# Performance work log

Hardware: AMD Instinct MI355X
Metric: run time of the kernel (lower is better)

Reference implementation:

```python
import jax, jax.numpy as jnp
import numpy as np

N_AGENTS = 10000
N_TARGETS = 10000
N_EDGES = 320000
IN_CH = 8
DS = 32          # n_channels // 2 per GAT preprocessor
NCH = 64         # n_channels
C = 128          # 2 * n_channels hidden width
OUT = 2
N_TAPS = 3
N_LAYERS = 2
RADIUS = 2.0
K_NBR = 10       # max_num_neighbors in radius_graph
BIG = 1e9


def radius_nbrs(qpos, kpos, radius, k, exclude_self):
    """For each query point, indices of <=k nearest key points within radius."""
    d2 = jnp.sum((qpos[:, None, :] - kpos[None, :, :]) ** 2, axis=-1)  # [Nq, Nk]
    if exclude_self:
        n = qpos.shape[0]
        d2 = d2.at[jnp.arange(n), jnp.arange(n)].set(BIG)
    d2 = jnp.where(d2 <= radius * radius, d2, BIG)
    negv, idx = jax.lax.top_k(-d2, k)   # nearest-k (deterministic stand-in for PyG's first-k)
    valid = negv > -BIG * 0.5           # [Nq, k] True where a real in-radius neighbor
    return idx, valid


def gatv2(src_feats, dst_feats, idx, valid, Wl, Wr, att, b):
    """Single-head GATv2Conv over a fixed-K neighbor list (idx indexes src_feats)."""
    xl = src_feats @ Wl                      # [Ns, H] messages
    xr = dst_feats @ Wr                      # [Nd, H]
    g = jax.nn.leaky_relu(xl[idx] + xr[:, None, :], 0.2)   # [Nd, K, H]
    s = jnp.einsum('nkh,h->nk', g, att)
    s = jnp.where(valid, s, -BIG)
    s = s - jnp.max(s, axis=1, keepdims=True)
    p = jnp.exp(s) * valid                   # masked exp; isolated nodes -> all-zero
    alpha = p / (jnp.sum(p, axis=1, keepdims=True) + 1e-16)
    return jnp.einsum('nk,nkh->nh', alpha, xl[idx]) + b


def graph_filter(x, src, dst, W, b, n):
    """Polynomial graph filter: y = sum_k S^k x W_k + b, S = unweighted adjacency."""
    y = x @ W[0]
    h = x
    for k in range(1, W.shape[0]):
        h = jax.ops.segment_sum(h[src], dst, num_segments=n)  # one shift tap
        y = y + h @ W[k]
    return y + b


def setup_inputs() -> dict:
    key = jax.random.key(0)
    ks = jax.random.split(key, 16)
    f32 = jnp.float32
    return {
        'own_obs': jax.random.normal(ks[0], (N_AGENTS, IN_CH), dtype=f32),
        'agent_positions': jax.random.uniform(ks[1], (N_AGENTS, 2), dtype=f32) * 100.0,
        'target_positions': jax.random.uniform(ks[2], (N_TARGETS, 2), dtype=f32) * 100.0,
        'W_self': jax.random.normal(ks[3], (IN_CH, NCH), dtype=f32) * 0.1,
        'b_self': jnp.zeros((NCH,), f32),
        'ag_Wl': jax.random.normal(ks[4], (2, DS), dtype=f32) * 0.1,
        'ag_Wr': jax.random.normal(ks[5], (2, DS), dtype=f32) * 0.1,
        'ag_att': jax.random.normal(ks[6], (DS,), dtype=f32) * 0.1,
        'ag_b': jnp.zeros((DS,), f32),
        'tg_Wl': jax.random.normal(ks[7], (2, DS), dtype=f32) * 0.1,
        'tg_Wr': jax.random.normal(ks[8], (2, DS), dtype=f32) * 0.1,
        'tg_att': jax.random.normal(ks[9], (DS,), dtype=f32) * 0.1,
        'tg_b': jnp.zeros((DS,), f32),
        'gf_W': jax.random.normal(ks[10], (N_LAYERS, N_TAPS + 1, C, C), dtype=f32) * (1.0 / np.sqrt(C)),
        'gf_b': jnp.zeros((N_LAYERS, C), f32),
        'bn_gamma': jnp.ones((N_LAYERS, C), f32),
        'bn_beta': jnp.zeros((N_LAYERS, C), f32),
        'W_read': jax.random.normal(ks[11], (C, OUT), dtype=f32) * 0.1,
        'b_read': jnp.zeros((OUT,), f32),
        'edge_index': jax.random.randint(ks[12], (2, N_EDGES), 0, N_AGENTS, dtype=jnp.int32),
    }


def reference(own_obs, agent_positions, target_positions, W_self, b_self,
              ag_Wl, ag_Wr, ag_att, ag_b, tg_Wl, tg_Wr, tg_att, tg_b,
              gf_W, gf_b, bn_gamma, bn_beta, W_read, b_read, edge_index):
    n = agent_positions.shape[0]
    # dynamic radius graphs (agent-agent; target->agent)
    a_idx, a_valid = radius_nbrs(agent_positions, agent_positions, RADIUS, K_NBR, True)
    t_idx, t_valid = radius_nbrs(agent_positions, target_positions, RADIUS, K_NBR, False)

    s = own_obs @ W_self + b_self                                            # self MLP (1 layer)
    a = gatv2(agent_positions, agent_positions, a_idx, a_valid, ag_Wl, ag_Wr, ag_att, ag_b)
    t = gatv2(target_positions, agent_positions, t_idx, t_valid, tg_Wl, tg_Wr, tg_att, tg_b)
    x = jnp.concatenate([s, a, t], axis=1)                                   # [N, 128]

    src, dst = edge_index[0], edge_index[1]
    for l in range(N_LAYERS):
        h = graph_filter(x, src, dst, gf_W[l], gf_b[l], n)
        mu = jnp.mean(h, axis=0)
        var = jnp.var(h, axis=0)
        h = (h - mu) / jnp.sqrt(var + 1e-5) * bn_gamma[l] + bn_beta[l]       # BatchNorm
        x = x + jax.nn.leaky_relu(h, 0.01)                                   # residual block
    return x @ W_read + b_read
```

## Files before the change

kernel.cpp:

```cpp
#include <hip/hip_runtime.h>

typedef unsigned long long u64;
typedef unsigned int u32;
typedef unsigned short ushort_t;

#define NA 10000
#define NE 320000
#define KN 10
#define GRID 50
#define NCELL (GRID * GRID)
#define GATB 157

typedef __attribute__((ext_vector_type(8))) short short8v;
typedef __attribute__((ext_vector_type(4))) float f32x4;

__device__ __forceinline__ u32 f2bf(float f) {
  union { float f; u32 u; } v; v.f = f;
  return (v.u + 0x7fffu + ((v.u >> 16) & 1u)) >> 16;
}
__device__ __forceinline__ float bf2f(u32 b) {
  union { u32 u; float f; } v; v.u = b << 16;
  return v.f;
}

__device__ __forceinline__ void insert10(u64* top, u64 key) {
#pragma unroll
  for (int t = 9; t > 0; --t) {
    u64 prev = top[t - 1];
    u64 cur = top[t];
    top[t] = (key < prev) ? prev : ((key < cur) ? key : cur);
  }
  top[0] = (key < top[0]) ? key : top[0];
}

__device__ __forceinline__ int cell_of(float2 p) {
  int cx = (int)(p.x * 0.5f);
  int cy = (int)(p.y * 0.5f);
  cx = min(max(cx, 0), GRID - 1);
  cy = min(max(cy, 0), GRID - 1);
  return cy * GRID + cx;
}

__global__ __launch_bounds__(256) void k_zero_packw(int* __restrict__ deg, int* __restrict__ cur,
                                                    int* __restrict__ chist, int* __restrict__ ccur,
                                                    const float* __restrict__ gfW,
                                                    ushort_t* __restrict__ Wh, ushort_t* __restrict__ Wlo) {
  int i = blockIdx.x * 256 + threadIdx.x;
  if (i < NA) deg[i] = 0;
  else if (i < 2 * NA) cur[i - NA] = 0;
  else if (i < 2 * NA + 2 * NCELL) chist[i - 2 * NA] = 0;
  else if (i < 2 * NA + 4 * NCELL) ccur[i - 2 * NA - 2 * NCELL] = 0;
  if (i < 131072) {
    int l = i >> 16;
    int rem = i & 65535;
    int t = rem >> 14;
    int k = (rem >> 7) & 127;
    int n = rem & 127;
    float v = gfW[(size_t)i];
    int kt = k >> 5;
    int hi = (k >> 3) & 3;
    int j = k & 7;
    int ct = n >> 4;
    int lane = hi * 16 + (n & 15);
    size_t dst = (((((size_t)(l * 4 + t) * 4 + kt) * 8 + ct) * 64 + lane) * 8 + j);
    u32 h = f2bf(v);
    float r = v - bf2f(h);
    Wh[dst] = (ushort_t)h;
    Wlo[dst] = (ushort_t)f2bf(r);
  }
}

__global__ __launch_bounds__(256) void k_hist_self(const int* __restrict__ edst,
                                                   const float2* __restrict__ apos,
                                                   const float2* __restrict__ tpos,
                                                   int* __restrict__ deg, int* __restrict__ chist,
                                                   const float* __restrict__ own_obs,
                                                   const float* __restrict__ W_self, const float* __restrict__ b_self,
                                                   float* __restrict__ x) {
  __shared__ float sW[512], sb[64];
  int t = threadIdx.x;
  for (int i = t; i < 512; i += 256) sW[i] = W_self[i];
  if (t < 64) sb[t] = b_self[t];
  __syncthreads();
  int i = blockIdx.x * 256 + t;
  if (i < NE) {
    atomicAdd(&deg[edst[i]], 1);
  } else if (i < NE + 2 * NA) {
    int ii = i - NE;
    int graph = (ii >= NA) ? 1 : 0;
    int idx = ii - graph * NA;
    float2 p = graph ? tpos[idx] : apos[idx];
    atomicAdd(&chist[graph * NCELL + cell_of(p)], 1);
  } else if (i < NE + 2 * NA + 8 * NA) {
    int gid = i - NE - 2 * NA;
    int q = gid >> 3;
    int c8 = (gid & 7) * 8;
    const float4* op = (const float4*)(own_obs + (size_t)q * 8);
    float4 o0 = op[0], o1 = op[1];
    float obs[8] = {o0.x, o0.y, o0.z, o0.w, o1.x, o1.y, o1.z, o1.w};
    float out[8];
#pragma unroll
    for (int jj = 0; jj < 8; ++jj) {
      int c = c8 + jj;
      float s = sb[c];
#pragma unroll
      for (int k = 0; k < 8; ++k) s += obs[k] * sW[k * 64 + c];
      out[jj] = s;
    }
    float* xrow = x + (size_t)q * 128 + c8;
    *(float4*)(xrow) = make_float4(out[0], out[1], out[2], out[3]);
    *(float4*)(xrow + 4) = make_float4(out[4], out[5], out[6], out[7]);
  }
}

__global__ __launch_bounds__(1024) void k_scan_all(const int* __restrict__ deg, int* __restrict__ rp,
                                                   const int* __restrict__ chist, int* __restrict__ crp) {
  __shared__ int part[1024];
  int t = threadIdx.x;
  const int* in;
  int* out;
  int per, tot;
  if (blockIdx.x == 0) { in = deg; out = rp; per = 10; tot = NA; }
  else { in = chist; out = crp; per = 5; tot = 2 * NCELL; }
  int beg = min(t * per, tot), end = min(beg + per, tot);
  int s = 0;
  for (int i = beg; i < end; ++i) s += in[i];
  part[t] = s;
  __syncthreads();
  for (int o = 1; o < 1024; o <<= 1) {
    int v = part[t];
    int u = (t >= o) ? part[t - o] : 0;
    __syncthreads();
    part[t] = v + u;
    __syncthreads();
  }
  int base = (t > 0) ? part[t - 1] : 0;
  for (int i = beg; i < end; ++i) { out[i] = base; base += in[i]; }
  if (t == 1023) out[tot] = part[1023];
}

__global__ __launch_bounds__(256) void k_scatter_all(const int* __restrict__ esrc, const int* __restrict__ edst,
                                                     const int* __restrict__ rp, int* __restrict__ cur,
                                                     int* __restrict__ col,
                                                     const float2* __restrict__ apos, const float2* __restrict__ tpos,
                                                     const int* __restrict__ crp, int* __restrict__ ccur,
                                                     float2* __restrict__ ps, int* __restrict__ pid) {
  int i = blockIdx.x * 256 + threadIdx.x;
  if (i < NE) {
    int d = edst[i];
    int p = atomicAdd(&cur[d], 1);
    col[rp[d] + p] = esrc[i];
  } else if (i < NE + 2 * NA) {
    int ii = i - NE;
    int graph = (ii >= NA) ? 1 : 0;
    int idx = ii - graph * NA;
    float2 p = graph ? tpos[idx] : apos[idx];
    int gc = graph * NCELL + cell_of(p);
    int o = crp[gc] + atomicAdd(&ccur[gc], 1);
    ps[o] = p;
    pid[o] = idx;
  }
}

__global__ __launch_bounds__(256) void k_nbr2(const float2* __restrict__ apos,
                                              const int* __restrict__ rp,
                                              const float2* __restrict__ ps, const int* __restrict__ pid,
                                              int* __restrict__ a_idx, int* __restrict__ a_cnt,
                                              int* __restrict__ t_idx, int* __restrict__ t_cnt) {
  int tid = blockIdx.x * 256 + threadIdx.x;
  if (tid >= 2 * NA) return;
  int graph = (tid >= NA) ? 1 : 0;
  int q = tid - graph * NA;
  float2 qp = apos[q];
  int cx = min(max((int)(qp.x * 0.5f), 0), GRID - 1);
  int cy = min(max((int)(qp.y * 0.5f), 0), GRID - 1);

  u64 top[10];
#pragma unroll
  for (int t = 0; t < 10; ++t) top[t] = ~0ull;

  int x0 = max(cx - 1, 0), x1 = min(cx + 1, GRID - 1);
  int y0 = max(cy - 1, 0), y1 = min(cy + 1, GRID - 1);
  for (int yy = y0; yy <= y1; ++yy) {
    int cb = graph * NCELL + yy * GRID + x0;
    int ce = graph * NCELL + yy * GRID + x1;
    int b = rp[cb], e = rp[ce + 1];
    for (int j = b; j < e; ++j) {
      float2 kp = ps[j];
      float dx = qp.x - kp.x;
      float dy = qp.y - kp.y;
      float d2 = __fadd_rn(__fmul_rn(dx, dx), __fmul_rn(dy, dy));
      int g = pid[j];
      if (d2 <= 4.0f && !(graph == 0 && g == q)) {
        u64 key = ((u64)__float_as_uint(d2) << 32) | (u32)g;
        if (key < top[9]) insert10(top, key);
      }
    }
  }
  int cnt = 0;
#pragma unroll
  for (int t = 0; t < 10; ++t) cnt += (top[t] != ~0ull) ? 1 : 0;
  int* oi = graph ? t_idx : a_idx;
#pragma unroll
  for (int t = 0; t < 10; ++t) oi[(size_t)q * 10 + t] = (int)(u32)(top[t] & 0xffffffffu);
  if (graph) t_cnt[q] = cnt; else a_cnt[q] = cnt;
}

__global__ __launch_bounds__(64) void k_gat2(const float2* __restrict__ apos, const float2* __restrict__ tpos,
                                             const int* __restrict__ a_idx, const int* __restrict__ a_cnt,
                                             const int* __restrict__ t_idx, const int* __restrict__ t_cnt,
                                             const float* __restrict__ agWl, const float* __restrict__ agWr,
                                             const float* __restrict__ agatt, const float* __restrict__ agb,
                                             const float* __restrict__ tgWl, const float* __restrict__ tgWr,
                                             const float* __restrict__ tgatt, const float* __restrict__ tgb,
                                             float* __restrict__ x) {
  int graph = (blockIdx.x >= GATB) ? 1 : 0;
  int b0 = blockIdx.x - graph * GATB;
  const float2* srcpos = graph ? tpos : apos;
  const int* idx_all = graph ? t_idx : a_idx;
  const int* cnt_all = graph ? t_cnt : a_cnt;
  const float* Wl = graph ? tgWl : agWl;
  const float* Wr = graph ? tgWr : agWr;
  const float* att = graph ? tgatt : agatt;
  const float* bbp = graph ? tgb : agb;
  int outoff = graph ? 96 : 64;

  __shared__ float sWl[64], sWr[64], satt[32], sbb[32];
  int t = threadIdx.x;
  sWl[t] = Wl[t];
  sWr[t] = Wr[t];
  if (t < 32) { satt[t] = att[t]; sbb[t] = bbp[t]; }
  __syncthreads();
  int q = b0 * 64 + t;
  if (q >= NA) return;
  float2 qp = apos[q];
  float xr[32];
#pragma unroll
  for (int c = 0; c < 32; ++c) xr[c] = qp.x * sWr[c] + qp.y * sWr[32 + c];
  const int* il = idx_all + (size_t)q * 10;
  int cnt = cnt_all[q];
  int idx[10];
#pragma unroll
  for (int k = 0; k < 10; ++k) idx[k] = (k < cnt) ? il[k] : 0;
  float pv[10];
  float m = -1e30f;
#pragma unroll
  for (int k = 0; k < 10; ++k) {
    float2 p = srcpos[idx[k]];
    float s = 0.f;
#pragma unroll
    for (int c = 0; c < 32; ++c) {
      float xl = p.x * sWl[c] + p.y * sWl[32 + c];
      float g = xl + xr[c];
      g = (g >= 0.f) ? g : 0.2f * g;
      s += satt[c] * g;
    }
    pv[k] = s;
    m = (k < cnt) ? fmaxf(m, s) : m;
  }
  float sum = 0.f;
#pragma unroll
  for (int k = 0; k < 10; ++k) {
    float e = (k < cnt) ? expf(pv[k] - m) : 0.f;
    pv[k] = e;
    sum += e;
  }
  float inv = 1.f / (sum + 1e-16f);
  float out[32];
#pragma unroll
  for (int c = 0; c < 32; ++c) out[c] = sbb[c];
#pragma unroll
  for (int k = 0; k < 10; ++k) {
    float a = pv[k] * inv;
    float2 p = srcpos[idx[k]];
#pragma unroll
    for (int c = 0; c < 32; ++c) {
      float xl = p.x * sWl[c] + p.y * sWl[32 + c];
      out[c] += a * xl;
    }
  }
  float* xrow = x + (size_t)q * 128 + outoff;
#pragma unroll
  for (int c4 = 0; c4 < 8; ++c4)
    *(float4*)(xrow + c4 * 4) = make_float4(out[c4 * 4], out[c4 * 4 + 1], out[c4 * 4 + 2], out[c4 * 4 + 3]);
}

__global__ __launch_bounds__(256) void k_shift3(const float* __restrict__ xin, float* __restrict__ xout,
                                                const int* __restrict__ rp, const int* __restrict__ col) {
  int bid = blockIdx.x;
  int half = (bid & 7) >> 2;
  int slot = (bid >> 3) * 4 + (bid & 3);
  if (slot >= 625) return;
  int wid = threadIdx.x >> 6;
  int lane = threadIdx.x & 63;
  int q = lane >> 4;
  int li = lane & 15;
  int row = slot * 16 + wid * 4 + q;
  int beg = rp[row], end = rp[row + 1];
  const f32x4* x4 = (const f32x4*)xin;
  int base = half * 16 + li;
  f32x4 acc = {0.f, 0.f, 0.f, 0.f};
  int j = beg;
  for (; j + 1 < end; j += 2) {
    int s0 = col[j], s1 = col[j + 1];
    f32x4 v0 = x4[(size_t)s0 * 32 + base];
    f32x4 v1 = x4[(size_t)s1 * 32 + base];
    acc += v0;
    acc += v1;
  }
  if (j < end) acc += x4[(size_t)col[j] * 32 + base];
  __builtin_nontemporal_store(acc, &((f32x4*)xout)[(size_t)row * 32 + base]);
}

__global__ __launch_bounds__(256) void k_gemm_mfma3(const float* __restrict__ a0, const float* __restrict__ a1,
                                                    const float* __restrict__ a2, const float* __restrict__ a3,
                                                    const ushort_t* __restrict__ Wh, const ushort_t* __restrict__ Wlo,
                                                    const float* __restrict__ b, float* __restrict__ y,
                                                    double* __restrict__ parts) {
  const int lane = threadIdx.x & 63;
  const int wave = threadIdx.x >> 6;
  const int ct0 = wave * 2;
  const int row = lane & 15;
  const int hi = lane >> 4;
  const int rb = blockIdx.x * 16;

  f32x4 acc[2];
#pragma unroll
  for (int c = 0; c < 2; ++c) {
    float bv = b[(ct0 + c) * 16 + row];
    acc[c][0] = bv; acc[c][1] = bv; acc[c][2] = bv; acc[c][3] = bv;
  }

  const float* aps[4] = {a0, a1, a2, a3};
#pragma unroll
  for (int t = 0; t < 4; ++t) {
    const float* at = aps[t];
#pragma unroll
    for (int kt = 0; kt < 4; ++kt) {
      const float* ap = at + (size_t)(rb + row) * 128 + kt * 32 + hi * 8;
      float4 fa = *(const float4*)(ap);
      float4 fb = *(const float4*)(ap + 4);
      float av[8] = {fa.x, fa.y, fa.z, fa.w, fb.x, fb.y, fb.z, fb.w};
      short8v ah, al;
#pragma unroll
      for (int j = 0; j < 8; ++j) {
        u32 h = f2bf(av[j]);
        float r = av[j] - bf2f(h);
        ah[j] = (short)h;
        al[j] = (short)f2bf(r);
      }
#pragma unroll
      for (int c = 0; c < 2; ++c) {
        size_t widx = ((((size_t)t * 4 + kt) * 8 + (ct0 + c)) * 64 + lane) * 8;
        short8v bh = *(const short8v*)(Wh + widx);
        short8v bl = *(const short8v*)(Wlo + widx);
        acc[c] = __builtin_amdgcn_mfma_f32_16x16x32_bf16(ah, bh, acc[c], 0, 0, 0);
        acc[c] = __builtin_amdgcn_mfma_f32_16x16x32_bf16(al, bh, acc[c], 0, 0, 0);
        acc[c] = __builtin_amdgcn_mfma_f32_16x16x32_bf16(ah, bl, acc[c], 0, 0, 0);
      }
    }
  }

#pragma unroll
  for (int c = 0; c < 2; ++c) {
#pragma unroll
    for (int r = 0; r < 4; ++r) {
      int grow = rb + hi * 4 + r;
      y[(size_t)grow * 128 + (ct0 + c) * 16 + row] = acc[c][r];
    }
  }

#pragma unroll
  for (int c = 0; c < 2; ++c) {
    double s = 0.0, ss = 0.0;
#pragma unroll
    for (int r = 0; r < 4; ++r) {
      double v = (double)acc[c][r];
      s += v;
      ss += v * v;
    }
    s += __shfl_xor(s, 16);
    ss += __shfl_xor(ss, 16);
    s += __shfl_xor(s, 32);
    ss += __shfl_xor(ss, 32);
    if (hi == 0) {
      int ch = (ct0 + c) * 16 + row;
      parts[(size_t)ch * 625 + blockIdx.x] = s;
      parts[(size_t)(128 + ch) * 625 + blockIdx.x] = ss;
    }
  }
}

__global__ __launch_bounds__(256) void k_bnfin(const double* __restrict__ parts,
                                               const float* __restrict__ gamma, const float* __restrict__ beta,
                                               float* __restrict__ AB) {
  __shared__ double s0[256], s1[256];
  int ch = blockIdx.x;
  int t = threadIdx.x;
  const double* ps = parts + (size_t)ch * 625;
  const double* pq = parts + (size_t)(128 + ch) * 625;
  double a = 0.0, b = 0.0;
  for (int i = t; i < 625; i += 256) { a += ps[i]; b += pq[i]; }
  s0[t] = a;
  s1[t] = b;
  __syncthreads();
  for (int o = 128; o > 0; o >>= 1) {
    if (t < o) { s0[t] += s0[t + o]; s1[t] += s1[t + o]; }
    __syncthreads();
  }
  if (t == 0) {
    double mu = s0[0] / (double)NA;
    double var = s1[0] / (double)NA - mu * mu;
    double rs = 1.0 / sqrt(var + 1e-5);
    AB[ch] = (float)rs * gamma[ch];
    AB[128 + ch] = beta[ch] - (float)(mu * rs) * gamma[ch];
  }
}

__global__ __launch_bounds__(256) void k_bnapply(const float* __restrict__ y, const float* __restrict__ AB,
                                                 const float* __restrict__ Wread, const float* __restrict__ bread,
                                                 float* __restrict__ x, float* __restrict__ out, int doread) {
  __shared__ float sAB[256], sWr[256];
  int t = threadIdx.x;
  sAB[t] = AB[t];
  sWr[t] = Wread[t];
  __syncthreads();
  const int n4 = NA * 32;
  for (int i = blockIdx.x * 256 + t; i < n4; i += gridDim.x * 256) {
    float4 yv = ((const float4*)y)[i];
    int c = (i & 31) * 4;
    float v0 = yv.x * sAB[c + 0] + sAB[128 + c + 0];
    float v1 = yv.y * sAB[c + 1] + sAB[128 + c + 1];
    float v2 = yv.z * sAB[c + 2] + sAB[128 + c + 2];
    float v3 = yv.w * sAB[c + 3] + sAB[128 + c + 3];
    v0 = (v0 >= 0.f) ? v0 : 0.01f * v0;
    v1 = (v1 >= 0.f) ? v1 : 0.01f * v1;
    v2 = (v2 >= 0.f) ? v2 : 0.01f * v2;
    v3 = (v3 >= 0.f) ? v3 : 0.01f * v3;
    float4 xv = ((float4*)x)[i];
    xv.x += v0; xv.y += v1; xv.z += v2; xv.w += v3;
    ((float4*)x)[i] = xv;
    if (doread) {
      float a0 = xv.x * sWr[(c + 0) * 2] + xv.y * sWr[(c + 1) * 2] + xv.z * sWr[(c + 2) * 2] + xv.w * sWr[(c + 3) * 2];
      float a1 = xv.x * sWr[(c + 0) * 2 + 1] + xv.y * sWr[(c + 1) * 2 + 1] + xv.z * sWr[(c + 2) * 2 + 1] + xv.w * sWr[(c + 3) * 2 + 1];
#pragma unroll
      for (int o = 1; o < 32; o <<= 1) {
        a0 += __shfl_xor(a0, o);
        a1 += __shfl_xor(a1, o);
      }
      if ((i & 31) == 0) {
        int row = i >> 5;
        out[row * 2 + 0] = a0 + bread[0];
        out[row * 2 + 1] = a1 + bread[1];
      }
    }
  }
}

extern "C" void kernel_launch(void* const* d_in, const int* in_sizes, int n_in,
                              void* d_out, int out_size, void* d_ws, size_t ws_size,
                              hipStream_t stream) {
  (void)in_sizes; (void)n_in; (void)out_size; (void)ws_size;
  const float* own_obs = (const float*)d_in[0];
  const float2* apos = (const float2*)d_in[1];
  const float2* tpos = (const float2*)d_in[2];
  const float* W_self = (const float*)d_in[3];
  const float* b_self = (const float*)d_in[4];
  const float* agWl = (const float*)d_in[5];
  const float* agWr = (const float*)d_in[6];
  const float* agatt = (const float*)d_in[7];
  const float* agb = (const float*)d_in[8];
  const float* tgWl = (const float*)d_in[9];
  const float* tgWr = (const float*)d_in[10];
  const float* tgatt = (const float*)d_in[11];
  const float* tgb = (const float*)d_in[12];
  const float* gfW = (const float*)d_in[13];
  const float* gfb = (const float*)d_in[14];
  const float* bng = (const float*)d_in[15];
  const float* bnb = (const float*)d_in[16];
  const float* Wread = (const float*)d_in[17];
  const float* bread = (const float*)d_in[18];
  const int* ei = (const int*)d_in[19];
  const int* esrc = ei;
  const int* edst = ei + NE;

  char* w = (char*)d_ws;
  size_t off = 0;
  auto take = [&](size_t bytes) -> void* {
    void* p = w + off;
    off += (bytes + 255) & ~(size_t)255;
    return p;
  };
  int* a_idx = (int*)take((size_t)NA * KN * 4);
  int* t_idx = (int*)take((size_t)NA * KN * 4);
  int* a_cnt = (int*)take((size_t)NA * 4);
  int* t_cnt = (int*)take((size_t)NA * 4);
  float* x = (float*)take((size_t)NA * 128 * 4);
  float* y = (float*)take((size_t)NA * 128 * 4);
  float* sh1 = (float*)take((size_t)NA * 128 * 4);
  float* sh2 = (float*)take((size_t)NA * 128 * 4);
  float* sh3 = (float*)take((size_t)NA * 128 * 4);
  ushort_t* Wh = (ushort_t*)take((size_t)131072 * 2);
  ushort_t* Wlo = (ushort_t*)take((size_t)131072 * 2);
  double* parts = (double*)take((size_t)256 * 625 * 8);
  float* AB = (float*)take(256 * 4);
  int* deg = (int*)take((size_t)NA * 4);
  int* cur = (int*)take((size_t)NA * 4);
  int* rp = (int*)take((size_t)(NA + 1) * 4);
  int* col = (int*)take((size_t)NE * 4);
  int* chist = (int*)take((size_t)2 * NCELL * 4);
  int* crp = (int*)take((size_t)(2 * NCELL + 1) * 4);
  int* ccur = (int*)take((size_t)2 * NCELL * 4);
  float2* ps = (float2*)take((size_t)2 * NA * 8);
  int* pid = (int*)take((size_t)2 * NA * 4);

  k_zero_packw<<<131072 / 256, 256, 0, stream>>>(deg, cur, chist, ccur, gfW, Wh, Wlo);
  k_hist_self<<<(NE + 2 * NA + 8 * NA + 255) / 256, 256, 0, stream>>>(edst, apos, tpos, deg, chist,
                                                                      own_obs, W_self, b_self, x);
  k_scan_all<<<2, 1024, 0, stream>>>(deg, rp, chist, crp);
  k_scatter_all<<<(NE + 2 * NA + 255) / 256, 256, 0, stream>>>(esrc, edst, rp, cur, col,
                                                               apos, tpos, crp, ccur, ps, pid);
  k_nbr2<<<(2 * NA + 255) / 256, 256, 0, stream>>>(apos, crp, ps, pid, a_idx, a_cnt, t_idx, t_cnt);
  k_gat2<<<2 * GATB, 64, 0, stream>>>(apos, tpos, a_idx, a_cnt, t_idx, t_cnt,
                                      agWl, agWr, agatt, agb, tgWl, tgWr, tgatt, tgb, x);

  for (int l = 0; l < 2; ++l) {
    const ushort_t* Whl = Wh + (size_t)l * 65536;
    const ushort_t* Wll = Wlo + (size_t)l * 65536;
    const float* bl = gfb + (size_t)l * 128;
    const float* gl = bng + (size_t)l * 128;
    const float* bb = bnb + (size_t)l * 128;
    k_shift3<<<1256, 256, 0, stream>>>(x, sh1, rp, col);
    k_shift3<<<1256, 256, 0, stream>>>(sh1, sh2, rp, col);
    k_shift3<<<1256, 256, 0, stream>>>(sh2, sh3, rp, col);
    k_gemm_mfma3<<<NA / 16, 256, 0, stream>>>(x, sh1, sh2, sh3, Whl, Wll, bl, y, parts);
    k_bnfin<<<128, 256, 0, stream>>>(parts, gl, bb, AB);
    k_bnapply<<<256, 256, 0, stream>>>(y, AB, Wread, bread, x, (float*)d_out, l == 1 ? 1 : 0);
  }
}
```

Before: 251.2 us.

## Fuse neighbor search with GATv2 and degree-sort rows for SpMM shifts

Merges the radius-neighbor search kernel and the GATv2 attention kernel into one, keeping the top-10 neighbor indices in registers so the a_idx/t_idx/cnt buffers are never written or read back. It also builds a degree-bucketed row permutation (histogram in a third scan block, scatter in the scatter kernel) so the sparse shift kernels process rows of similar degree together and reduce wave divergence. The shift inner loop is unrolled to four gathers per iteration. The permutation costs extra atomics and an indirect row lookup, and the fused kernel uses more registers, which may lower occupancy.

```diff
diff --git a/kernel.cpp b/kernel.cpp
--- a/kernel.cpp
+++ b/kernel.cpp
@@ -9,7 +9,6 @@
 #define KN 10
 #define GRID 50
 #define NCELL (GRID * GRID)
-#define GATB 157
 
 typedef __attribute__((ext_vector_type(8))) short short8v;
 typedef __attribute__((ext_vector_type(4))) float f32x4;
@@ -43,6 +42,7 @@
 
 __global__ __launch_bounds__(256) void k_zero_packw(int* __restrict__ deg, int* __restrict__ cur,
                                                     int* __restrict__ chist, int* __restrict__ ccur,
+                                                    int* __restrict__ dcur,
                                                     const float* __restrict__ gfW,
                                                     ushort_t* __restrict__ Wh, ushort_t* __restrict__ Wlo) {
   int i = blockIdx.x * 256 + threadIdx.x;
@@ -50,6 +50,7 @@
   else if (i < 2 * NA) cur[i - NA] = 0;
   else if (i < 2 * NA + 2 * NCELL) chist[i - 2 * NA] = 0;
   else if (i < 2 * NA + 4 * NCELL) ccur[i - 2 * NA - 2 * NCELL] = 0;
+  else if (i < 2 * NA + 4 * NCELL + 128) dcur[i - 2 * NA - 4 * NCELL] = 0;
   if (i < 131072) {
     int l = i >> 16;
     int rem = i & 65535;
@@ -114,9 +115,22 @@
 }
 
 __global__ __launch_bounds__(1024) void k_scan_all(const int* __restrict__ deg, int* __restrict__ rp,
-                                                   const int* __restrict__ chist, int* __restrict__ crp) {
+                                                   const int* __restrict__ chist, int* __restrict__ crp,
+                                                   int* __restrict__ dbase) {
+  int t = threadIdx.x;
+  if (blockIdx.x == 2) {
+    __shared__ int dh[128];
+    if (t < 128) dh[t] = 0;
+    __syncthreads();
+    for (int i = t; i < NA; i += 1024) atomicAdd(&dh[min(deg[i], 127)], 1);
+    __syncthreads();
+    if (t == 0) {
+      int run = 0;
+      for (int b = 0; b < 128; ++b) { int c = dh[b]; dbase[b] = run; run += c; }
+    }
+    return;
+  }
   __shared__ int part[1024];
-  int t = threadIdx.x;
   const int* in;
   int* out;
   int per, tot;
@@ -144,7 +158,9 @@
                                                      int* __restrict__ col,
                                                      const float2* __restrict__ apos, const float2* __restrict__ tpos,
                                                      const int* __restrict__ crp, int* __restrict__ ccur,
-                                                     float2* __restrict__ ps, int* __restrict__ pid) {
+                                                     float2* __restrict__ ps, int* __restrict__ pid,
+                                                     const int* __restrict__ deg, const int* __restrict__ dbase,
+                                                     int* __restrict__ dcur, int* __restrict__ perm) {
   int i = blockIdx.x * 256 + threadIdx.x;
   if (i < NE) {
     int d = edst[i];
@@ -159,15 +175,31 @@
     int o = crp[gc] + atomicAdd(&ccur[gc], 1);
     ps[o] = p;
     pid[o] = idx;
-  }
-}
-
-__global__ __launch_bounds__(256) void k_nbr2(const float2* __restrict__ apos,
-                                              const int* __restrict__ rp,
-                                              const float2* __restrict__ ps, const int* __restrict__ pid,
-                                              int* __restrict__ a_idx, int* __restrict__ a_cnt,
-                                              int* __restrict__ t_idx, int* __restrict__ t_cnt) {
-  int tid = blockIdx.x * 256 + threadIdx.x;
+  } else if (i < NE + 2 * NA + NA) {
+    int r = i - NE - 2 * NA;
+    int b = min(deg[r], 127);
+    int pos = atomicAdd(&dcur[b], 1);
+    perm[dbase[b] + pos] = r;
+  }
+}
+
+__global__ __launch_bounds__(256) void k_nbr_gat(const float2* __restrict__ apos, const float2* __restrict__ tpos,
+                                                 const int* __restrict__ crp,
+                                                 const float2* __restrict__ ps, const int* __restrict__ pid,
+                                                 const float* __restrict__ agWl, const float* __restrict__ agWr,
+                                                 const float* __restrict__ agatt, const float* __restrict__ agb,
+                                                 const float* __restrict__ tgWl, const float* __restrict__ tgWr,
+                                                 const float* __restrict__ tgatt, const float* __restrict__ tgb,
+                                                 float* __restrict__ x) {
+  __shared__ float sWl[2][64], sWr[2][64], satt[2][32], sbb[2][32];
+  int t = threadIdx.x;
+  if (t < 64) { sWl[0][t] = agWl[t]; sWr[0][t] = agWr[t]; sWl[1][t] = tgWl[t]; sWr[1][t] = tgWr[t]; }
+  else if (t < 96) {
+    int u = t - 64;
+    satt[0][u] = agatt[u]; sbb[0][u] = agb[u]; satt[1][u] = tgatt[u]; sbb[1][u] = tgb[u];
+  }
+  __syncthreads();
+  int tid = blockIdx.x * 256 + t;
   if (tid >= 2 * NA) return;
   int graph = (tid >= NA) ? 1 : 0;
   int q = tid - graph * NA;
@@ -177,14 +209,14 @@
 
   u64 top[10];
 #pragma unroll
-  for (int t = 0; t < 10; ++t) top[t] = ~0ull;
+  for (int k = 0; k < 10; ++k) top[k] = ~0ull;
 
   int x0 = max(cx - 1, 0), x1 = min(cx + 1, GRID - 1);
   int y0 = max(cy - 1, 0), y1 = min(cy + 1, GRID - 1);
   for (int yy = y0; yy <= y1; ++yy) {
     int cb = graph * NCELL + yy * GRID + x0;
     int ce = graph * NCELL + yy * GRID + x1;
-    int b = rp[cb], e = rp[ce + 1];
+    int b = crp[cb], e = crp[ce + 1];
     for (int j = b; j < e; ++j) {
       float2 kp = ps[j];
       float dx = qp.x - kp.x;
@@ -199,49 +231,19 @@
   }
   int cnt = 0;
 #pragma unroll
-  for (int t = 0; t < 10; ++t) cnt += (top[t] != ~0ull) ? 1 : 0;
-  int* oi = graph ? t_idx : a_idx;
-#pragma unroll
-  for (int t = 0; t < 10; ++t) oi[(size_t)q * 10 + t] = (int)(u32)(top[t] & 0xffffffffu);
-  if (graph) t_cnt[q] = cnt; else a_cnt[q] = cnt;
-}
-
-__global__ __launch_bounds__(64) void k_gat2(const float2* __restrict__ apos, const float2* __restrict__ tpos,
-                                             const int* __restrict__ a_idx, const int* __restrict__ a_cnt,
-                                             const int* __restrict__ t_idx, const int* __restrict__ t_cnt,
-                                             const float* __restrict__ agWl, const float* __restrict__ agWr,
-                                             const float* __restrict__ agatt, const float* __restrict__ agb,
-                                             const float* __restrict__ tgWl, const float* __restrict__ tgWr,
-                                             const float* __restrict__ tgatt, const float* __restrict__ tgb,
-                                             float* __restrict__ x) {
-  int graph = (blockIdx.x >= GATB) ? 1 : 0;
-  int b0 = blockIdx.x - graph * GATB;
+  for (int k = 0; k < 10; ++k) cnt += (top[k] != ~0ull) ? 1 : 0;
+  int idx[10];
+#pragma unroll
+  for (int k = 0; k < 10; ++k) idx[k] = (k < cnt) ? (int)(u32)(top[k] & 0xffffffffu) : 0;
+
   const float2* srcpos = graph ? tpos : apos;
-  const int* idx_all = graph ? t_idx : a_idx;
-  const int* cnt_all = graph ? t_cnt : a_cnt;
-  const float* Wl = graph ? tgWl : agWl;
-  const float* Wr = graph ? tgWr : agWr;
-  const float* att = graph ? tgatt : agatt;
-  const float* bbp = graph ? tgb : agb;
-  int outoff = graph ? 96 : 64;
-
-  __shared__ float sWl[64], sWr[64], satt[32], sbb[32];
-  int t = threadIdx.x;
-  sWl[t] = Wl[t];
-  sWr[t] = Wr[t];
-  if (t < 32) { satt[t] = att[t]; sbb[t] = bbp[t]; }
-  __syncthreads();
-  int q = b0 * 64 + t;
-  if (q >= NA) return;
-  float2 qp = apos[q];
+  const float* wl = sWl[graph];
+  const float* wr = sWr[graph];
+  const float* at = satt[graph];
+  const float* bb = sbb[graph];
   float xr[32];
 #pragma unroll
-  for (int c = 0; c < 32; ++c) xr[c] = qp.x * sWr[c] + qp.y * sWr[32 + c];
-  const int* il = idx_all + (size_t)q * 10;
-  int cnt = cnt_all[q];
-  int idx[10];
-#pragma unroll
-  for (int k = 0; k < 10; ++k) idx[k] = (k < cnt) ? il[k] : 0;
+  for (int c = 0; c < 32; ++c) xr[c] = qp.x * wr[c] + qp.y * wr[32 + c];
   float pv[10];
   float m = -1e30f;
 #pragma unroll
@@ -250,10 +252,10 @@
     float s = 0.f;
 #pragma unroll
     for (int c = 0; c < 32; ++c) {
-      float xl = p.x * sWl[c] + p.y * sWl[32 + c];
+      float xl = p.x * wl[c] + p.y * wl[32 + c];
       float g = xl + xr[c];
       g = (g >= 0.f) ? g : 0.2f * g;
-      s += satt[c] * g;
+      s += at[c] * g;
     }
     pv[k] = s;
     m = (k < cnt) ? fmaxf(m, s) : m;
@@ -268,25 +270,26 @@
   float inv = 1.f / (sum + 1e-16f);
   float out[32];
 #pragma unroll
-  for (int c = 0; c < 32; ++c) out[c] = sbb[c];
+  for (int c = 0; c < 32; ++c) out[c] = bb[c];
 #pragma unroll
   for (int k = 0; k < 10; ++k) {
     float a = pv[k] * inv;
     float2 p = srcpos[idx[k]];
 #pragma unroll
     for (int c = 0; c < 32; ++c) {
-      float xl = p.x * sWl[c] + p.y * sWl[32 + c];
+      float xl = p.x * wl[c] + p.y * wl[32 + c];
       out[c] += a * xl;
     }
   }
-  float* xrow = x + (size_t)q * 128 + outoff;
+  float* xrow = x + (size_t)q * 128 + (graph ? 96 : 64);
 #pragma unroll
   for (int c4 = 0; c4 < 8; ++c4)
     *(float4*)(xrow + c4 * 4) = make_float4(out[c4 * 4], out[c4 * 4 + 1], out[c4 * 4 + 2], out[c4 * 4 + 3]);
 }
 
 __global__ __launch_bounds__(256) void k_shift3(const float* __restrict__ xin, float* __restrict__ xout,
-                                                const int* __restrict__ rp, const int* __restrict__ col) {
+                                                const int* __restrict__ rp, const int* __restrict__ col,
+                                                const int* __restrict__ perm) {
   int bid = blockIdx.x;
   int half = (bid & 7) >> 2;
   int slot = (bid >> 3) * 4 + (bid & 3);
@@ -295,20 +298,24 @@
   int lane = threadIdx.x & 63;
   int q = lane >> 4;
   int li = lane & 15;
-  int row = slot * 16 + wid * 4 + q;
+  int row = perm[slot * 16 + wid * 4 + q];
   int beg = rp[row], end = rp[row + 1];
   const f32x4* x4 = (const f32x4*)xin;
   int base = half * 16 + li;
   f32x4 acc = {0.f, 0.f, 0.f, 0.f};
   int j = beg;
-  for (; j + 1 < end; j += 2) {
-    int s0 = col[j], s1 = col[j + 1];
+  for (; j + 3 < end; j += 4) {
+    int s0 = col[j], s1 = col[j + 1], s2 = col[j + 2], s3 = col[j + 3];
     f32x4 v0 = x4[(size_t)s0 * 32 + base];
     f32x4 v1 = x4[(size_t)s1 * 32 + base];
+    f32x4 v2 = x4[(size_t)s2 * 32 + base];
+    f32x4 v3 = x4[(size_t)s3 * 32 + base];
     acc += v0;
     acc += v1;
-  }
-  if (j < end) acc += x4[(size_t)col[j] * 32 + base];
+    acc += v2;
+    acc += v3;
+  }
+  for (; j < end; ++j) acc += x4[(size_t)col[j] * 32 + base];
   __builtin_nontemporal_store(acc, &((f32x4*)xout)[(size_t)row * 32 + base]);
 }
 
@@ -491,10 +498,6 @@
     off += (bytes + 255) & ~(size_t)255;
     return p;
   };
-  int* a_idx = (int*)take((size_t)NA * KN * 4);
-  int* t_idx = (int*)take((size_t)NA * KN * 4);
-  int* a_cnt = (int*)take((size_t)NA * 4);
-  int* t_cnt = (int*)take((size_t)NA * 4);
   float* x = (float*)take((size_t)NA * 128 * 4);
   float* y = (float*)take((size_t)NA * 128 * 4);
   float* sh1 = (float*)take((size_t)NA * 128 * 4);
@@ -513,16 +516,19 @@
   int* ccur = (int*)take((size_t)2 * NCELL * 4);
   float2* ps = (float2*)take((size_t)2 * NA * 8);
   int* pid = (int*)take((size_t)2 * NA * 4);
-
-  k_zero_packw<<<131072 / 256, 256, 0, stream>>>(deg, cur, chist, ccur, gfW, Wh, Wlo);
+  int* dbase = (int*)take(128 * 4);
+  int* dcur = (int*)take(128 * 4);
+  int* perm = (int*)take((size_t)NA * 4);
+
+  k_zero_packw<<<131072 / 256, 256, 0, stream>>>(deg, cur, chist, ccur, dcur, gfW, Wh, Wlo);
   k_hist_self<<<(NE + 2 * NA + 8 * NA + 255) / 256, 256, 0, stream>>>(edst, apos, tpos, deg, chist,
                                                                       own_obs, W_self, b_self, x);
-  k_scan_all<<<2, 1024, 0, stream>>>(deg, rp, chist, crp);
-  k_scatter_all<<<(NE + 2 * NA + 255) / 256, 256, 0, stream>>>(esrc, edst, rp, cur, col,
-                                                               apos, tpos, crp, ccur, ps, pid);
-  k_nbr2<<<(2 * NA + 255) / 256, 256, 0, stream>>>(apos, crp, ps, pid, a_idx, a_cnt, t_idx, t_cnt);
-  k_gat2<<<2 * GATB, 64, 0, stream>>>(apos, tpos, a_idx, a_cnt, t_idx, t_cnt,
-                                      agWl, agWr, agatt, agb, tgWl, tgWr, tgatt, tgb, x);
+  k_scan_all<<<3, 1024, 0, stream>>>(deg, rp, chist, crp, dbase);
+  k_scatter_all<<<(NE + 3 * NA + 255) / 256, 256, 0, stream>>>(esrc, edst, rp, cur, col,
+                                                               apos, tpos, crp, ccur, ps, pid,
+                                                               deg, dbase, dcur, perm);
+  k_nbr_gat<<<(2 * NA + 255) / 256, 256, 0, stream>>>(apos, tpos, crp, ps, pid,
+                                                      agWl, agWr, agatt, agb, tgWl, tgWr, tgatt, tgb, x);
 
   for (int l = 0; l < 2; ++l) {
     const ushort_t* Whl = Wh + (size_t)l * 65536;
@@ -530,9 +536,9 @@
     const float* bl = gfb + (size_t)l * 128;
     const float* gl = bng + (size_t)l * 128;
     const float* bb = bnb + (size_t)l * 128;
-    k_shift3<<<1256, 256, 0, stream>>>(x, sh1, rp, col);
-    k_shift3<<<1256, 256, 0, stream>>>(sh1, sh2, rp, col);
-    k_shift3<<<1256, 256, 0, stream>>>(sh2, sh3, rp, col);
+    k_shift3<<<1256, 256, 0, stream>>>(x, sh1, rp, col, perm);
+    k_shift3<<<1256, 256, 0, stream>>>(sh1, sh2, rp, col, perm);
+    k_shift3<<<1256, 256, 0, stream>>>(sh2, sh3, rp, col, perm);
     k_gemm_mfma3<<<NA / 16, 256, 0, stream>>>(x, sh1, sh2, sh3, Whl, Wll, bl, y, parts);
     k_bnfin<<<128, 256, 0, stream>>>(parts, gl, bb, AB);
     k_bnapply<<<256, 256, 0, stream>>>(y, AB, Wread, bread, x, (float*)d_out, l == 1 ? 1 : 0);
```

Measured after the change: 254.4 us. Within noise of the previous version (+1.3%).
